# Performance work log

Measured on AMD Instinct MI355X. Metric: run time of the kernel, lower is better.

Reference implementation:

```python
import jax, jax.numpy as jnp
import numpy as np

N, E, G = 100000, 300000, 4096
ND, ED, H, ZI, ZS, NE, L = 64, 16, 256, 128, 128, 8, 3
LAMBDA_GRL = 1.0


def setup_inputs() -> dict:
    key = jax.random.key(0)
    ks = iter(jax.random.split(key, 64))
    def nrm(shape, scale=0.05):
        return jax.random.normal(next(ks), shape, jnp.float32) * scale
    inp = {
        'x': jax.random.normal(next(ks), (N, ND), jnp.float32),
        'edge_index': jax.random.randint(next(ks), (2, E), 0, N),
        'edge_attr': jax.random.normal(next(ks), (E, ED), jnp.float32),
        'batch': jnp.sort(jax.random.randint(next(ks), (N,), 0, G)),
        'node_W': nrm((ND, H)), 'node_b': nrm((H,)),
        'conv_eps': jnp.zeros((L,), jnp.float32),
        'edge_W': nrm((L, ED, H)), 'edge_b': nrm((L, H)),
        'mlp_W1': nrm((L, H, H)), 'mlp_b1': nrm((L, H)),
        'mlp_W2': nrm((L, H, H)), 'mlp_b2': nrm((L, H)),
        'gn_w': jnp.ones((L, H), jnp.float32), 'gn_b': jnp.zeros((L, H), jnp.float32),
        'gn_ms': jnp.ones((L, H), jnp.float32),
        'finv_W1': nrm((H, ZI)), 'finv_b1': nrm((ZI,)),
        'finv_W2': nrm((ZI, ZI)), 'finv_b2': nrm((ZI,)),
        'fspu_W1': nrm((H, ZS)), 'fspu_b1': nrm((ZS,)),
        'fspu_W2': nrm((ZS, ZS)), 'fspu_b2': nrm((ZS,)),
        'pred_W1': nrm((ZI, ZI)), 'pred_b1': nrm((ZI,)),
        'pred_W2': nrm((ZI, 1)), 'pred_b2': nrm((1,)),
        'adv_W1': nrm((ZI, ZI)), 'adv_b1': nrm((ZI,)),
        'adv_W2': nrm((ZI, NE)), 'adv_b2': nrm((NE,)),
    }
    return inp


def _mlp2(h, W1, b1, W2, b2):
    return jax.nn.relu(h @ W1 + b1) @ W2 + b2


def reference(x, edge_index, edge_attr, batch, node_W, node_b, conv_eps,
              edge_W, edge_b, mlp_W1, mlp_b1, mlp_W2, mlp_b2,
              gn_w, gn_b, gn_ms,
              finv_W1, finv_b1, finv_W2, finv_b2,
              fspu_W1, fspu_b1, fspu_W2, fspu_b2,
              pred_W1, pred_b1, pred_W2, pred_b2,
              adv_W1, adv_b1, adv_W2, adv_b2):
    src, dst = edge_index[0], edge_index[1]
    cnt = jax.ops.segment_sum(jnp.ones((N, 1), jnp.float32), batch, num_segments=G)
    cnt = jnp.maximum(cnt, 1.0)
    h = x @ node_W + node_b  # [N,H]
    for l in range(L):
        # GINEConv: sum_j relu(x_j + lin(e_ij))
        e = edge_attr @ edge_W[l] + edge_b[l]            # [E,H]
        m = jax.nn.relu(h[src] + e)                      # [E,H]
        agg = jax.ops.segment_sum(m, dst, num_segments=N)
        h = _mlp2((1.0 + conv_eps[l]) * h + agg, mlp_W1[l], mlp_b1[l], mlp_W2[l], mlp_b2[l])
        # GraphNorm
        mean = jax.ops.segment_sum(h, batch, num_segments=G) / cnt  # [G,H]
        out = h - gn_ms[l] * mean[batch]
        var = jax.ops.segment_sum(out * out, batch, num_segments=G) / cnt
        h = out * jax.lax.rsqrt(var[batch] + 1e-5) * gn_w[l] + gn_b[l]
        h = jax.nn.relu(h)  # dropout is identity at eval
    hg = jax.ops.segment_sum(h, batch, num_segments=G) / cnt  # global_mean_pool [G,H]
    z_inv = _mlp2(hg, finv_W1, finv_b1, finv_W2, finv_b2)
    z_spu = _mlp2(hg, fspu_W1, fspu_b1, fspu_W2, fspu_b2)
    yhat = _mlp2(z_inv, pred_W1, pred_b1, pred_W2, pred_b2)[:, 0]
    # gradient reversal: identity fwd, -lambda on bwd
    grl = jax.lax.stop_gradient(z_inv) * (1.0 + LAMBDA_GRL) - LAMBDA_GRL * z_inv
    envhat = _mlp2(grl, adv_W1, adv_b1, adv_W2, adv_b2)
    return (hg, z_inv, z_spu, yhat, envhat)
```

## Files before the change

kernel.cpp:

```cpp
#include <hip/hip_runtime.h>
#include <hip/hip_bf16.h>

typedef __bf16 bf16_t;
typedef __bf16 bf16x8 __attribute__((ext_vector_type(8)));
typedef __bf16 bf16x4 __attribute__((ext_vector_type(4)));
typedef float  f32x4  __attribute__((ext_vector_type(4)));

static constexpr int N_NODES = 100000;
static constexpr int N_EDGES = 300000;
static constexpr int N_GRAPH = 4096;
static constexpr int H  = 256;
static constexpr int ND = 64;
static constexpr int ZIC = 128;
static constexpr int NE = 8;
static constexpr int SCAN_B = 1024;

__device__ __forceinline__ int clampi(int v, int lo, int hi) {
  return v < lo ? lo : (v > hi ? hi : v);
}

__device__ __forceinline__ void dma16(const bf16_t* g, bf16_t* lds_base) {
  __builtin_amdgcn_global_load_lds(
      (const __attribute__((address_space(1))) void*)g,
      (__attribute__((address_space(3))) void*)lds_base, 16, 0, 0);
}

__global__ void compute_starts_kernel(const int* __restrict__ batch,
                                      int* __restrict__ starts, int N, int G) {
  int i = blockIdx.x * blockDim.x + threadIdx.x;
  if (i >= N) return;
  int b = clampi(batch[i], 0, G - 1);
  if (i == 0) {
    for (int g = 0; g <= b; ++g) starts[g] = 0;
  } else {
    int p = clampi(batch[i - 1], 0, G - 1);
    for (int g = p + 1; g <= b; ++g) starts[g] = i;
  }
  if (i == N - 1) {
    for (int g = b + 1; g <= G; ++g) starts[g] = N;
  }
}

__global__ void zero2_kernel(int* __restrict__ a, int* __restrict__ b, int N) {
  int i = blockIdx.x * blockDim.x + threadIdx.x;
  if (i < N) { a[i] = 0; b[i] = 0; }
}

__global__ void count_deg_kernel(const int* __restrict__ dst, int* __restrict__ counts, int E, int N) {
  int e = blockIdx.x * blockDim.x + threadIdx.x;
  if (e < E) atomicAdd(&counts[clampi(dst[e], 0, N - 1)], 1);
}

__global__ __launch_bounds__(SCAN_B) void scan1_kernel(const int* __restrict__ counts,
                                                       int* __restrict__ offs,
                                                       int* __restrict__ bsum, int N) {
  __shared__ int tmp[SCAN_B];
  int i = blockIdx.x * SCAN_B + threadIdx.x;
  int v = (i < N) ? counts[i] : 0;
  tmp[threadIdx.x] = v;
  __syncthreads();
  for (int d = 1; d < SCAN_B; d <<= 1) {
    int t = (threadIdx.x >= d) ? tmp[threadIdx.x - d] : 0;
    __syncthreads();
    tmp[threadIdx.x] += t;
    __syncthreads();
  }
  if (i < N) offs[i + 1] = tmp[threadIdx.x];
  if (threadIdx.x == SCAN_B - 1) bsum[blockIdx.x] = tmp[SCAN_B - 1];
  if (i == 0) offs[0] = 0;
}

__global__ void scan2_kernel(int* __restrict__ bsum, int nblk) {
  if (blockIdx.x == 0 && threadIdx.x == 0) {
    int run = 0;
    for (int b = 0; b < nblk; ++b) { int v = bsum[b]; bsum[b] = run; run += v; }
  }
}

__global__ __launch_bounds__(SCAN_B) void scan3_kernel(int* __restrict__ offs,
                                                       const int* __restrict__ bsum, int N) {
  int i = blockIdx.x * SCAN_B + threadIdx.x;
  if (i < N) offs[i + 1] += bsum[blockIdx.x];
}

__global__ void fill_perm_kernel(const int* __restrict__ dst, const int* __restrict__ offs,
                                 int* __restrict__ cursor, int* __restrict__ perm, int E, int N) {
  int e = blockIdx.x * blockDim.x + threadIdx.x;
  if (e >= E) return;
  int d = clampi(dst[e], 0, N - 1);
  int pos = offs[d] + atomicAdd(&cursor[d], 1);
  if ((unsigned)pos < (unsigned)E) perm[pos] = e;
}

__global__ void sort_src_kernel(const int* __restrict__ perm, const int* __restrict__ src,
                                int* __restrict__ src_sorted, int E) {
  int p = blockIdx.x * blockDim.x + threadIdx.x;
  if (p >= E) return;
  int e = perm[p];
  e = ((unsigned)e < (unsigned)E) ? e : 0;
  int s = src[e];
  src_sorted[p] = ((unsigned)s < (unsigned)N_NODES) ? s : 0;
}

__global__ void build_eattr16_kernel(const float* __restrict__ eattr,
                                     const int* __restrict__ perm,
                                     bf16_t* __restrict__ ep, int E) {
  int idx = blockIdx.x * blockDim.x + threadIdx.x;
  if (idx >= E * 16) return;
  int p = idx >> 4, k = idx & 15;
  int e = perm[p];
  e = ((unsigned)e < (unsigned)E) ? e : 0;
  ep[idx] = (bf16_t)eattr[(size_t)e * 16 + k];
}

__global__ void build_ewt16_kernel(const float* __restrict__ edge_W,
                                   bf16_t* __restrict__ ewt) {
  int idx = blockIdx.x * blockDim.x + threadIdx.x;
  if (idx >= 3 * 256 * 16) return;
  int l = idx / (256 * 16);
  int rem = idx - l * 256 * 16;
  int n = rem >> 4, k = rem & 15;
  ewt[idx] = (bf16_t)edge_W[(size_t)l * 16 * 256 + k * 256 + n];
}

__global__ void transpose_kernel(const float* __restrict__ W,
                                 bf16_t* __restrict__ Wt, int K, int Nc) {
  __shared__ float tile[32][33];
  int n0 = blockIdx.x * 32, k0 = blockIdx.y * 32;
  int tx = threadIdx.x, ty = threadIdx.y;
  for (int i = ty; i < 32; i += 8)
    tile[i][tx] = W[(size_t)(k0 + i) * Nc + n0 + tx];
  __syncthreads();
  for (int i = ty; i < 32; i += 8)
    Wt[(size_t)(n0 + i) * K + k0 + tx] = (bf16_t)tile[tx][i];
}

__device__ __forceinline__ void load8_to_lds(const bf16_t* p, bool valid, uint4* dst) {
  uint4 v = make_uint4(0u, 0u, 0u, 0u);
  if (valid) v = *(const uint4*)p;
  *dst = v;
}
__device__ __forceinline__ void load8_to_lds(const float* p, bool valid, uint4* dst) {
  float4 f0 = make_float4(0.f, 0.f, 0.f, 0.f), f1 = f0;
  if (valid) { f0 = *(const float4*)p; f1 = *(const float4*)(p + 4); }
  union { bf16_t b[8]; uint4 u; } pk;
  pk.b[0] = (bf16_t)f0.x; pk.b[1] = (bf16_t)f0.y;
  pk.b[2] = (bf16_t)f0.z; pk.b[3] = (bf16_t)f0.w;
  pk.b[4] = (bf16_t)f1.x; pk.b[5] = (bf16_t)f1.y;
  pk.b[6] = (bf16_t)f1.z; pk.b[7] = (bf16_t)f1.w;
  *dst = pk.u;
}

template<int K, bool RELU, bool OUTF32, typename TIN>
__global__ __launch_bounds__(256) void gemm128_kernel(
    const TIN* __restrict__ U, const bf16_t* __restrict__ Wt,
    const float* __restrict__ bias, void* __restrict__ Out, int M, int Nc) {
  constexpr int LDT = 72;
  __shared__ bf16_t Ut[128 * LDT];
  __shared__ bf16_t Wl[128 * LDT];
  const int m0 = blockIdx.x * 128;
  const int n0 = blockIdx.y * 128;
  const int t = threadIdx.x;
  const int lane = t & 63;
  const int wave = t >> 6;
  const int wm = (wave >> 1) * 64;
  const int wn = (wave & 1) * 64;
  const int srow = t >> 1;
  const int sk = (t & 1) * 32;
  const int lr = lane & 15;
  const int lq = lane >> 4;
  const bool aok = (m0 + srow) < M;
  f32x4 acc[4][4] = {};

  for (int k0 = 0; k0 < K; k0 += 64) {
    const TIN* up = U + (size_t)(m0 + srow) * K + k0 + sk;
    const bf16_t* wp = Wt + (size_t)(n0 + srow) * K + k0 + sk;
#pragma unroll
    for (int q = 0; q < 4; ++q) {
      load8_to_lds(up + q * 8, aok, (uint4*)&Ut[srow * LDT + sk + q * 8]);
      load8_to_lds(wp + q * 8, true, (uint4*)&Wl[srow * LDT + sk + q * 8]);
    }
    __syncthreads();
#pragma unroll
    for (int s = 0; s < 2; ++s) {
      bf16x8 a[4], b[4];
#pragma unroll
      for (int mt = 0; mt < 4; ++mt)
        a[mt] = *(const bf16x8*)(&Ut[(wm + mt * 16 + lr) * LDT + s * 32 + lq * 8]);
#pragma unroll
      for (int nt = 0; nt < 4; ++nt)
        b[nt] = *(const bf16x8*)(&Wl[(wn + nt * 16 + lr) * LDT + s * 32 + lq * 8]);
#pragma unroll
      for (int mt = 0; mt < 4; ++mt)
#pragma unroll
        for (int nt = 0; nt < 4; ++nt)
          acc[mt][nt] = __builtin_amdgcn_mfma_f32_16x16x32_bf16(
              a[mt], b[nt], acc[mt][nt], 0, 0, 0);
    }
    __syncthreads();
  }

#pragma unroll
  for (int mt = 0; mt < 4; ++mt)
#pragma unroll
    for (int nt = 0; nt < 4; ++nt) {
      int col = n0 + wn + nt * 16 + lr;
      float bcol = bias[col];
#pragma unroll
      for (int r = 0; r < 4; ++r) {
        int row = m0 + wm + mt * 16 + lq * 4 + r;
        if (row < M) {
          float vv = acc[mt][nt][r] + bcol;
          if (RELU) vv = vv > 0.f ? vv : 0.f;
          if (OUTF32) ((float*)Out)[(size_t)row * Nc + col] = vv;
          else        ((bf16_t*)Out)[(size_t)row * Nc + col] = (bf16_t)vv;
        }
      }
    }
}

template<int K, bool RELU, bool OUTF32, typename TIN>
__global__ __launch_bounds__(256) void gemm64_kernel(
    const TIN* __restrict__ U, const bf16_t* __restrict__ Wt,
    const float* __restrict__ bias, void* __restrict__ Out, int M, int Nc) {
  constexpr int LDT = 72;
  __shared__ bf16_t Ut[64 * LDT];
  __shared__ bf16_t Wl[64 * LDT];
  const int m0 = blockIdx.x * 64;
  const int n0 = blockIdx.y * 64;
  const int t = threadIdx.x;
  const int lane = t & 63;
  const int wave = t >> 6;
  const int wm = (wave >> 1) * 32;
  const int wn = (wave & 1) * 32;
  const int srow = t >> 2;
  const int sk = (t & 3) * 8;
  const int lr = lane & 15;
  const int lq = lane >> 4;
  const bool aok = (m0 + srow) < M;
  f32x4 acc[2][2] = {};

  for (int k0 = 0; k0 < K; k0 += 64) {
    const TIN* up = U + (size_t)(m0 + srow) * K + k0 + sk;
    const bf16_t* wp = Wt + (size_t)(n0 + srow) * K + k0 + sk;
    load8_to_lds(up,      aok, (uint4*)&Ut[srow * LDT + sk]);
    load8_to_lds(up + 32, aok, (uint4*)&Ut[srow * LDT + sk + 32]);
    load8_to_lds(wp,      true, (uint4*)&Wl[srow * LDT + sk]);
    load8_to_lds(wp + 32, true, (uint4*)&Wl[srow * LDT + sk + 32]);
    __syncthreads();
#pragma unroll
    for (int s = 0; s < 2; ++s) {
      bf16x8 a[2], b[2];
#pragma unroll
      for (int mt = 0; mt < 2; ++mt)
        a[mt] = *(const bf16x8*)(&Ut[(wm + mt * 16 + lr) * LDT + s * 32 + lq * 8]);
#pragma unroll
      for (int nt = 0; nt < 2; ++nt)
        b[nt] = *(const bf16x8*)(&Wl[(wn + nt * 16 + lr) * LDT + s * 32 + lq * 8]);
#pragma unroll
      for (int mt = 0; mt < 2; ++mt)
#pragma unroll
        for (int nt = 0; nt < 2; ++nt)
          acc[mt][nt] = __builtin_amdgcn_mfma_f32_16x16x32_bf16(
              a[mt], b[nt], acc[mt][nt], 0, 0, 0);
    }
    __syncthreads();
  }

#pragma unroll
  for (int mt = 0; mt < 2; ++mt)
#pragma unroll
    for (int nt = 0; nt < 2; ++nt) {
      int col = n0 + wn + nt * 16 + lr;
      float bcol = bias[col];
#pragma unroll
      for (int r = 0; r < 4; ++r) {
        int row = m0 + wm + mt * 16 + lq * 4 + r;
        if (row < M) {
          float vv = acc[mt][nt][r] + bcol;
          if (RELU) vv = vv > 0.f ? vv : 0.f;
          if (OUTF32) ((float*)Out)[(size_t)row * Nc + col] = vv;
          else        ((bf16_t*)Out)[(size_t)row * Nc + col] = (bf16_t)vv;
        }
      }
    }
}

template<int K, bool RELU, bool OUTF32>
__global__ __launch_bounds__(256) void gemm128_dma_kernel(
    const bf16_t* __restrict__ U, const bf16_t* __restrict__ Wt,
    const float* __restrict__ bias, void* __restrict__ Out, int M, int Nc) {
  __shared__ bf16_t Ut[128 * 64];
  __shared__ bf16_t Wl[128 * 64];
  const int t = threadIdx.x;
  const int lane = t & 63;
  const int wave = t >> 6;
  const int m0 = blockIdx.x * 128;
  const int n0 = blockIdx.y * 128;
  const int wm = (wave >> 1) * 64;
  const int wn = (wave & 1) * 64;
  const int lr = lane & 15;
  const int lq = lane >> 4;
  const int subrow = wave * 8 + (lane >> 3);
  const int lchunk = (lane & 7) ^ (lane >> 3);
  f32x4 acc[4][4] = {};

  for (int k0 = 0; k0 < K; k0 += 64) {
#pragma unroll
    for (int q = 0; q < 4; ++q) {
      const int row = q * 32 + subrow;
      int urow = m0 + row; if (urow >= M) urow = M - 1;
      dma16(U + (size_t)urow * K + k0 + lchunk * 8, &Ut[(q * 32 + wave * 8) * 64]);
      dma16(Wt + (size_t)(n0 + row) * K + k0 + lchunk * 8, &Wl[(q * 32 + wave * 8) * 64]);
    }
    __syncthreads();
#pragma unroll
    for (int s = 0; s < 2; ++s) {
      bf16x8 a[4], b[4];
#pragma unroll
      for (int mt = 0; mt < 4; ++mt)
        a[mt] = *(const bf16x8*)(&Ut[(wm + mt * 16 + lr) * 64 + (((s * 4 + lq) ^ (lr & 7)) << 3)]);
#pragma unroll
      for (int nt = 0; nt < 4; ++nt)
        b[nt] = *(const bf16x8*)(&Wl[(wn + nt * 16 + lr) * 64 + (((s * 4 + lq) ^ (lr & 7)) << 3)]);
#pragma unroll
      for (int mt = 0; mt < 4; ++mt)
#pragma unroll
        for (int nt = 0; nt < 4; ++nt)
          acc[mt][nt] = __builtin_amdgcn_mfma_f32_16x16x32_bf16(
              a[mt], b[nt], acc[mt][nt], 0, 0, 0);
    }
    __syncthreads();
  }

#pragma unroll
  for (int mt = 0; mt < 4; ++mt)
#pragma unroll
    for (int nt = 0; nt < 4; ++nt) {
      int col = n0 + wn + nt * 16 + lr;
      float bcol = bias[col];
#pragma unroll
      for (int r = 0; r < 4; ++r) {
        int row = m0 + wm + mt * 16 + lq * 4 + r;
        if (row < M) {
          float vv = acc[mt][nt][r] + bcol;
          if (RELU) vv = vv > 0.f ? vv : 0.f;
          if (OUTF32) ((float*)Out)[(size_t)row * Nc + col] = vv;
          else        ((bf16_t*)Out)[(size_t)row * Nc + col] = (bf16_t)vv;
        }
      }
    }
}

__global__ __launch_bounds__(256) void gine_gather_mfma_kernel(
    const bf16_t* __restrict__ h, const bf16_t* __restrict__ eat16,
    const int* __restrict__ src_sorted, const int* __restrict__ offs,
    const bf16_t* __restrict__ ewt, const float* __restrict__ eb,
    const float* __restrict__ eps_p, bf16_t* __restrict__ u) {
  constexpr int HP = H + 8;
  __shared__ bf16_t slin[2][16 * HP];
  const int t = threadIdx.x;
  const int wave = t >> 6;
  const int lane = t & 63;
  const int lr = lane & 15;
  const int lq = lane >> 4;
  const int lane4 = lane * 4;
  const int n0 = blockIdx.x * 4;
  const int nodeN = n0 + wave;

  bf16x4 hs = *(const bf16x4*)(h + (size_t)nodeN * H + lane4);

  bf16x8 bfrag[4];
#pragma unroll
  for (int nt = 0; nt < 4; ++nt) {
    bf16x8 bv = {};
    if (lq < 2)
      bv = *(const bf16x8*)(ewt + ((wave * 64 + nt * 16 + lr) << 4) + (lq << 3));
    bfrag[nt] = bv;
  }
  float ebv[4];
#pragma unroll
  for (int i = 0; i < 4; ++i) ebv[i] = eb[lane4 + i];

  int bs = offs[n0], be = offs[n0 + 4];
  bs = clampi(bs, 0, N_EDGES);
  be = clampi(be, bs, N_EDGES);
  int ns = offs[nodeN], ne = offs[nodeN + 1];
  ns = clampi(ns, bs, be);
  ne = clampi(ne, ns, be);

  float acc[4] = {0.f, 0.f, 0.f, 0.f};
  int parity = 0;

  for (int cb = bs; cb < be; cb += 16, parity ^= 1) {
    int arow = cb + lr;
    if (arow >= N_EDGES) arow = N_EDGES - 1;
    bf16x8 afrag = {};
    if (lq < 2)
      afrag = *(const bf16x8*)(eat16 + ((size_t)arow << 4) + (lq << 3));
    f32x4 c[4];
#pragma unroll
    for (int nt = 0; nt < 4; ++nt) {
      f32x4 z = {};
      c[nt] = __builtin_amdgcn_mfma_f32_16x16x32_bf16(afrag, bfrag[nt], z, 0, 0, 0);
    }
#pragma unroll
    for (int nt = 0; nt < 4; ++nt)
#pragma unroll
      for (int r = 0; r < 4; ++r)
        slin[parity][(lq * 4 + r) * HP + wave * 64 + nt * 16 + lr] = (bf16_t)c[nt][r];
    __syncthreads();
    int j0 = ns > cb ? ns : cb;
    int j1 = ne < cb + 16 ? ne : cb + 16;
    for (int jb = j0; jb < j1; jb += 4) {
      int sidx[4];
#pragma unroll
      for (int q = 0; q < 4; ++q) {
        int jj = jb + q; if (jj > j1 - 1) jj = j1 - 1;
        sidx[q] = src_sorted[jj];
      }
      bf16x4 hv[4];
#pragma unroll
      for (int q = 0; q < 4; ++q)
        hv[q] = *(const bf16x4*)(h + (size_t)sidx[q] * H + lane4);
#pragma unroll
      for (int q = 0; q < 4; ++q) {
        if (jb + q < j1) {
          bf16x4 lv = *(const bf16x4*)(&slin[parity][(jb + q - cb) * HP + lane4]);
#pragma unroll
          for (int i = 0; i < 4; ++i)
            acc[i] += fmaxf((float)hv[q][i] + (float)lv[i] + ebv[i], 0.f);
        }
      }
    }
  }

  const float sc = 1.0f + eps_p[0];
  union { bf16x4 v; uint2 b; } o;
#pragma unroll
  for (int i = 0; i < 4; ++i) o.v[i] = (bf16_t)(sc * (float)hs[i] + acc[i]);
  *(uint2*)(u + (size_t)nodeN * H + lane4) = o.b;
}

__global__ __launch_bounds__(64) void graphnorm_kernel(
    const bf16_t* __restrict__ v, bf16_t* __restrict__ hout,
    const int* __restrict__ starts,
    const float* __restrict__ w, const float* __restrict__ b,
    const float* __restrict__ ms, float* __restrict__ hg) {
  const int g = blockIdx.x;
  const int c0 = threadIdx.x * 4;
  int s = starts[g], e = starts[g + 1];
  s = clampi(s, 0, N_NODES);
  e = clampi(e, s, N_NODES);
  const float cnt = (float)((e - s) > 1 ? (e - s) : 1);
  float sx[4] = {0.f, 0.f, 0.f, 0.f}, sxx[4] = {0.f, 0.f, 0.f, 0.f};
  for (int i = s; i < e; ++i) {
    bf16x4 xv = *(const bf16x4*)(v + (size_t)i * H + c0);
#pragma unroll
    for (int j = 0; j < 4; ++j) { float f = (float)xv[j]; sx[j] += f; sxx[j] += f * f; }
  }
  float sub[4], inv[4], bb[4], psum[4] = {0.f, 0.f, 0.f, 0.f};
#pragma unroll
  for (int j = 0; j < 4; ++j) {
    float mean = sx[j] / cnt;
    sub[j] = ms[c0 + j] * mean;
    float var = sxx[j] / cnt - 2.f * sub[j] * mean + sub[j] * sub[j];
    var = fmaxf(var, 0.f);
    inv[j] = rsqrtf(var + 1e-5f) * w[c0 + j];
    bb[j] = b[c0 + j];
  }
  for (int i = s; i < e; ++i) {
    bf16x4 xv = *(const bf16x4*)(v + (size_t)i * H + c0);
    union { bf16x4 o; uint2 u; } pk;
#pragma unroll
    for (int j = 0; j < 4; ++j) {
      float o = ((float)xv[j] - sub[j]) * inv[j] + bb[j];
      o = o > 0.f ? o : 0.f;
      psum[j] += o;
      pk.o[j] = (bf16_t)o;
    }
    *(uint2*)(hout + (size_t)i * H + c0) = pk.u;
  }
  if (hg) {
#pragma unroll
    for (int j = 0; j < 4; ++j) hg[(size_t)g * H + c0 + j] = psum[j] / cnt;
  }
}

__global__ void head_out_kernel(const bf16_t* __restrict__ In, const float* __restrict__ W,
                                const float* __restrict__ bias, float* __restrict__ Out,
                                int M, int K, int Nc) {
  int idx = blockIdx.x * blockDim.x + threadIdx.x;
  if (idx >= M * Nc) return;
  int r = idx / Nc, n = idx - r * Nc;
  float acc = bias[n];
  const bf16_t* in = In + (size_t)r * K;
  for (int k = 0; k < K; ++k) acc += (float)in[k] * W[(size_t)k * Nc + n];
  Out[idx] = acc;
}

extern "C" void kernel_launch(void* const* d_in, const int* in_sizes, int n_in,
                              void* d_out, int out_size, void* d_ws, size_t ws_size,
                              hipStream_t stream) {
  (void)in_sizes; (void)n_in; (void)out_size; (void)ws_size;
  const float* x        = (const float*)d_in[0];
  const int*   eidx     = (const int*)d_in[1];
  const float* eattr    = (const float*)d_in[2];
  const int*   batch    = (const int*)d_in[3];
  const float* node_W   = (const float*)d_in[4];
  const float* node_b   = (const float*)d_in[5];
  const float* conv_eps = (const float*)d_in[6];
  const float* edge_W   = (const float*)d_in[7];
  const float* edge_b   = (const float*)d_in[8];
  const float* mlp_W1   = (const float*)d_in[9];
  const float* mlp_b1   = (const float*)d_in[10];
  const float* mlp_W2   = (const float*)d_in[11];
  const float* mlp_b2   = (const float*)d_in[12];
  const float* gn_w     = (const float*)d_in[13];
  const float* gn_b     = (const float*)d_in[14];
  const float* gn_ms    = (const float*)d_in[15];
  const float* finv_W1  = (const float*)d_in[16];
  const float* finv_b1  = (const float*)d_in[17];
  const float* finv_W2  = (const float*)d_in[18];
  const float* finv_b2  = (const float*)d_in[19];
  const float* fspu_W1  = (const float*)d_in[20];
  const float* fspu_b1  = (const float*)d_in[21];
  const float* fspu_W2  = (const float*)d_in[22];
  const float* fspu_b2  = (const float*)d_in[23];
  const float* pred_W1  = (const float*)d_in[24];
  const float* pred_b1  = (const float*)d_in[25];
  const float* pred_W2  = (const float*)d_in[26];
  const float* pred_b2  = (const float*)d_in[27];
  const float* adv_W1   = (const float*)d_in[28];
  const float* adv_b1   = (const float*)d_in[29];
  const float* adv_W2   = (const float*)d_in[30];
  const float* adv_b2   = (const float*)d_in[31];
  float* out = (float*)d_out;

  float* out_hg = out;
  float* out_zi = out + (size_t)N_GRAPH * H;
  float* out_zs = out_zi + (size_t)N_GRAPH * ZIC;
  float* out_yh = out_zs + (size_t)N_GRAPH * ZIC;
  float* out_ev = out_yh + N_GRAPH;

  char* wp = (char*)d_ws;
  auto alloc = [&](size_t bytes) { char* p = wp; wp += (bytes + 255) & ~(size_t)255; return p; };
  bf16_t* A        = (bf16_t*)alloc((size_t)N_NODES * H * 2);
  bf16_t* B        = (bf16_t*)alloc((size_t)N_NODES * H * 2);
  bf16_t* Wt       = (bf16_t*)alloc((size_t)(H * ND + 6 * H * H) * 2);
  bf16_t* WtH      = (bf16_t*)alloc((size_t)(2 * ZIC * H + 4 * ZIC * ZIC) * 2);
  bf16_t* ewt16    = (bf16_t*)alloc((size_t)3 * 256 * 16 * 2);
  bf16_t* eat16    = (bf16_t*)alloc((size_t)N_EDGES * 16 * 2);
  int*    starts   = (int*)alloc((size_t)(N_GRAPH + 1) * 4);
  int*    counts   = (int*)alloc((size_t)N_NODES * 4);
  int*    cursor   = (int*)alloc((size_t)N_NODES * 4);
  int*    offs     = (int*)alloc((size_t)(N_NODES + 1) * 4);
  int*    bsum     = (int*)alloc((size_t)SCAN_B * 4);
  int*    perm     = (int*)alloc((size_t)N_EDGES * 4);
  int*    src_srt  = (int*)alloc((size_t)N_EDGES * 4);
  bf16_t* tmp1     = (bf16_t*)alloc((size_t)N_GRAPH * ZIC * 2);
  bf16_t* tmp2     = (bf16_t*)alloc((size_t)N_GRAPH * ZIC * 2);

  const int* srcp = eidx;
  const int* dstp = eidx + N_EDGES;
  const int nscan = (N_NODES + SCAN_B - 1) / SCAN_B;

  compute_starts_kernel<<<(N_NODES + 255) / 256, 256, 0, stream>>>(batch, starts, N_NODES, N_GRAPH);

  zero2_kernel<<<(N_NODES + 255) / 256, 256, 0, stream>>>(counts, cursor, N_NODES);
  count_deg_kernel<<<(N_EDGES + 255) / 256, 256, 0, stream>>>(dstp, counts, N_EDGES, N_NODES);
  scan1_kernel<<<nscan, SCAN_B, 0, stream>>>(counts, offs, bsum, N_NODES);
  scan2_kernel<<<1, 64, 0, stream>>>(bsum, nscan);
  scan3_kernel<<<nscan, SCAN_B, 0, stream>>>(offs, bsum, N_NODES);
  fill_perm_kernel<<<(N_EDGES + 255) / 256, 256, 0, stream>>>(dstp, offs, cursor, perm, N_EDGES, N_NODES);
  sort_src_kernel<<<(N_EDGES + 255) / 256, 256, 0, stream>>>(perm, srcp, src_srt, N_EDGES);
  build_eattr16_kernel<<<(N_EDGES * 16 + 255) / 256, 256, 0, stream>>>(eattr, perm, eat16, N_EDGES);
  build_ewt16_kernel<<<(3 * 256 * 16 + 255) / 256, 256, 0, stream>>>(edge_W, ewt16);

  bf16_t* WtN = Wt;
  auto Wt1l = [&](int l) { return Wt + H * ND + (size_t)(2 * l) * H * H; };
  auto Wt2l = [&](int l) { return Wt + H * ND + (size_t)(2 * l + 1) * H * H; };
  transpose_kernel<<<dim3(H / 32, ND / 32), dim3(32, 8), 0, stream>>>(node_W, WtN, ND, H);
  for (int l = 0; l < 3; ++l) {
    transpose_kernel<<<dim3(H / 32, H / 32), dim3(32, 8), 0, stream>>>(mlp_W1 + (size_t)l * H * H, Wt1l(l), H, H);
    transpose_kernel<<<dim3(H / 32, H / 32), dim3(32, 8), 0, stream>>>(mlp_W2 + (size_t)l * H * H, Wt2l(l), H, H);
  }
  bf16_t* fT1 = WtH;
  bf16_t* fT2 = fT1 + ZIC * H;
  bf16_t* sT1 = fT2 + ZIC * ZIC;
  bf16_t* sT2 = sT1 + ZIC * H;
  bf16_t* pT1 = sT2 + ZIC * ZIC;
  bf16_t* aT1 = pT1 + ZIC * ZIC;
  transpose_kernel<<<dim3(ZIC / 32, H / 32), dim3(32, 8), 0, stream>>>(finv_W1, fT1, H, ZIC);
  transpose_kernel<<<dim3(ZIC / 32, ZIC / 32), dim3(32, 8), 0, stream>>>(finv_W2, fT2, ZIC, ZIC);
  transpose_kernel<<<dim3(ZIC / 32, H / 32), dim3(32, 8), 0, stream>>>(fspu_W1, sT1, H, ZIC);
  transpose_kernel<<<dim3(ZIC / 32, ZIC / 32), dim3(32, 8), 0, stream>>>(fspu_W2, sT2, ZIC, ZIC);
  transpose_kernel<<<dim3(ZIC / 32, ZIC / 32), dim3(32, 8), 0, stream>>>(pred_W1, pT1, ZIC, ZIC);
  transpose_kernel<<<dim3(ZIC / 32, ZIC / 32), dim3(32, 8), 0, stream>>>(adv_W1, aT1, ZIC, ZIC);

  dim3 ggrid((N_NODES + 127) / 128, H / 128);
  gemm128_kernel<ND, false, false><<<ggrid, 256, 0, stream>>>(x, WtN, node_b, A, N_NODES, H);

  for (int l = 0; l < 3; ++l) {
    gine_gather_mfma_kernel<<<N_NODES / 4, 256, 0, stream>>>(
        A, eat16, src_srt, offs, ewt16 + (size_t)l * 256 * 16,
        edge_b + l * H, conv_eps + l, B);
    gemm128_dma_kernel<H, true,  false><<<ggrid, 256, 0, stream>>>(B, Wt1l(l), mlp_b1 + l * H, A, N_NODES, H);
    gemm128_dma_kernel<H, false, false><<<ggrid, 256, 0, stream>>>(A, Wt2l(l), mlp_b2 + l * H, B, N_NODES, H);
    graphnorm_kernel<<<N_GRAPH, 64, 0, stream>>>(B, A, starts, gn_w + l * H, gn_b + l * H,
                                                 gn_ms + l * H, (l == 2) ? out_hg : nullptr);
  }

  dim3 hgrid(N_GRAPH / 64, ZIC / 64);
  gemm64_kernel<H,   true,  false, float ><<<hgrid, 256, 0, stream>>>(out_hg, fT1, finv_b1, tmp1, N_GRAPH, ZIC);
  gemm64_kernel<ZIC, false, true,  bf16_t><<<hgrid, 256, 0, stream>>>(tmp1, fT2, finv_b2, out_zi, N_GRAPH, ZIC);
  gemm64_kernel<H,   true,  false, float ><<<hgrid, 256, 0, stream>>>(out_hg, sT1, fspu_b1, tmp2, N_GRAPH, ZIC);
  gemm64_kernel<ZIC, false, true,  bf16_t><<<hgrid, 256, 0, stream>>>(tmp2, sT2, fspu_b2, out_zs, N_GRAPH, ZIC);
  gemm64_kernel<ZIC, true,  false, float ><<<hgrid, 256, 0, stream>>>(out_zi, pT1, pred_b1, tmp1, N_GRAPH, ZIC);
  gemm64_kernel<ZIC, true,  false, float ><<<hgrid, 256, 0, stream>>>(out_zi, aT1, adv_b1, tmp2, N_GRAPH, ZIC);
  head_out_kernel<<<(N_GRAPH + 255) / 256, 256, 0, stream>>>(tmp1, pred_W2, pred_b2, out_yh, N_GRAPH, ZIC, 1);
  head_out_kernel<<<(N_GRAPH * NE + 255) / 256, 256, 0, stream>>>(tmp2, adv_W2, adv_b2, out_ev, N_GRAPH, ZIC, NE);
}
```

Before: 854.7 us.

## Fuse edge sort scatter kernels, batch weight transposes, unroll graphnorm loops

The three CSR-build kernels (perm fill, src gather, edge-attr gather) become one kernel that writes src and bf16 edge attributes directly at the sorted position. This removes the perm buffer and two launches. The per-layer weight transposes are batched into single launches over blockIdx.z. Graphnorm's two row loops are unrolled by four so several loads are in flight per thread. The atomic ordering within a node's edge segment is nondeterministic in both versions, so results are unchanged.

```diff
diff --git a/kernel.cpp b/kernel.cpp
--- a/kernel.cpp
+++ b/kernel.cpp
@@ -83,34 +83,25 @@
   if (i < N) offs[i + 1] += bsum[blockIdx.x];
 }
 
-__global__ void fill_perm_kernel(const int* __restrict__ dst, const int* __restrict__ offs,
-                                 int* __restrict__ cursor, int* __restrict__ perm, int E, int N) {
+__global__ void fill_scatter_kernel(const int* __restrict__ src, const int* __restrict__ dst,
+                                    const float* __restrict__ eattr,
+                                    const int* __restrict__ offs, int* __restrict__ cursor,
+                                    int* __restrict__ src_srt, bf16_t* __restrict__ eat16,
+                                    int E, int N) {
   int e = blockIdx.x * blockDim.x + threadIdx.x;
   if (e >= E) return;
   int d = clampi(dst[e], 0, N - 1);
   int pos = offs[d] + atomicAdd(&cursor[d], 1);
-  if ((unsigned)pos < (unsigned)E) perm[pos] = e;
-}
-
-__global__ void sort_src_kernel(const int* __restrict__ perm, const int* __restrict__ src,
-                                int* __restrict__ src_sorted, int E) {
-  int p = blockIdx.x * blockDim.x + threadIdx.x;
-  if (p >= E) return;
-  int e = perm[p];
-  e = ((unsigned)e < (unsigned)E) ? e : 0;
+  if ((unsigned)pos >= (unsigned)E) return;
   int s = src[e];
-  src_sorted[p] = ((unsigned)s < (unsigned)N_NODES) ? s : 0;
-}
-
-__global__ void build_eattr16_kernel(const float* __restrict__ eattr,
-                                     const int* __restrict__ perm,
-                                     bf16_t* __restrict__ ep, int E) {
-  int idx = blockIdx.x * blockDim.x + threadIdx.x;
-  if (idx >= E * 16) return;
-  int p = idx >> 4, k = idx & 15;
-  int e = perm[p];
-  e = ((unsigned)e < (unsigned)E) ? e : 0;
-  ep[idx] = (bf16_t)eattr[(size_t)e * 16 + k];
+  src_srt[pos] = ((unsigned)s < (unsigned)N_NODES) ? s : 0;
+  const float* ea = eattr + (size_t)e * 16;
+  union { bf16_t b[16]; uint4 u[2]; } pk;
+#pragma unroll
+  for (int k = 0; k < 16; ++k) pk.b[k] = (bf16_t)ea[k];
+  uint4* dst16 = (uint4*)(eat16 + ((size_t)pos << 4));
+  dst16[0] = pk.u[0];
+  dst16[1] = pk.u[1];
 }
 
 __global__ void build_ewt16_kernel(const float* __restrict__ edge_W,
@@ -124,15 +115,18 @@
 }
 
 __global__ void transpose_kernel(const float* __restrict__ W,
-                                 bf16_t* __restrict__ Wt, int K, int Nc) {
+                                 bf16_t* __restrict__ Wt, int K, int Nc,
+                                 size_t srcStride, size_t dstStride) {
   __shared__ float tile[32][33];
+  const float* Wz = W + (size_t)blockIdx.z * srcStride;
+  bf16_t* Wtz = Wt + (size_t)blockIdx.z * dstStride;
   int n0 = blockIdx.x * 32, k0 = blockIdx.y * 32;
   int tx = threadIdx.x, ty = threadIdx.y;
   for (int i = ty; i < 32; i += 8)
-    tile[i][tx] = W[(size_t)(k0 + i) * Nc + n0 + tx];
+    tile[i][tx] = Wz[(size_t)(k0 + i) * Nc + n0 + tx];
   __syncthreads();
   for (int i = ty; i < 32; i += 8)
-    Wt[(size_t)(n0 + i) * K + k0 + tx] = (bf16_t)tile[tx][i];
+    Wtz[(size_t)(n0 + i) * K + k0 + tx] = (bf16_t)tile[tx][i];
 }
 
 __device__ __forceinline__ void load8_to_lds(const bf16_t* p, bool valid, uint4* dst) {
@@ -454,7 +448,18 @@
   e = clampi(e, s, N_NODES);
   const float cnt = (float)((e - s) > 1 ? (e - s) : 1);
   float sx[4] = {0.f, 0.f, 0.f, 0.f}, sxx[4] = {0.f, 0.f, 0.f, 0.f};
-  for (int i = s; i < e; ++i) {
+  int i = s;
+  for (; i + 4 <= e; i += 4) {
+    bf16x4 xv[4];
+#pragma unroll
+    for (int q = 0; q < 4; ++q)
+      xv[q] = *(const bf16x4*)(v + (size_t)(i + q) * H + c0);
+#pragma unroll
+    for (int q = 0; q < 4; ++q)
+#pragma unroll
+      for (int j = 0; j < 4; ++j) { float f = (float)xv[q][j]; sx[j] += f; sxx[j] += f * f; }
+  }
+  for (; i < e; ++i) {
     bf16x4 xv = *(const bf16x4*)(v + (size_t)i * H + c0);
 #pragma unroll
     for (int j = 0; j < 4; ++j) { float f = (float)xv[j]; sx[j] += f; sxx[j] += f * f; }
@@ -469,7 +474,26 @@
     inv[j] = rsqrtf(var + 1e-5f) * w[c0 + j];
     bb[j] = b[c0 + j];
   }
-  for (int i = s; i < e; ++i) {
+  i = s;
+  for (; i + 4 <= e; i += 4) {
+    bf16x4 xv[4];
+#pragma unroll
+    for (int q = 0; q < 4; ++q)
+      xv[q] = *(const bf16x4*)(v + (size_t)(i + q) * H + c0);
+#pragma unroll
+    for (int q = 0; q < 4; ++q) {
+      union { bf16x4 o; uint2 u; } pk;
+#pragma unroll
+      for (int j = 0; j < 4; ++j) {
+        float o = ((float)xv[q][j] - sub[j]) * inv[j] + bb[j];
+        o = o > 0.f ? o : 0.f;
+        psum[j] += o;
+        pk.o[j] = (bf16_t)o;
+      }
+      *(uint2*)(hout + (size_t)(i + q) * H + c0) = pk.u;
+    }
+  }
+  for (; i < e; ++i) {
     bf16x4 xv = *(const bf16x4*)(v + (size_t)i * H + c0);
     union { bf16x4 o; uint2 u; } pk;
 #pragma unroll
@@ -556,7 +580,6 @@
   int*    cursor   = (int*)alloc((size_t)N_NODES * 4);
   int*    offs     = (int*)alloc((size_t)(N_NODES + 1) * 4);
   int*    bsum     = (int*)alloc((size_t)SCAN_B * 4);
-  int*    perm     = (int*)alloc((size_t)N_EDGES * 4);
   int*    src_srt  = (int*)alloc((size_t)N_EDGES * 4);
   bf16_t* tmp1     = (bf16_t*)alloc((size_t)N_GRAPH * ZIC * 2);
   bf16_t* tmp2     = (bf16_t*)alloc((size_t)N_GRAPH * ZIC * 2);
@@ -572,31 +595,33 @@
   scan1_kernel<<<nscan, SCAN_B, 0, stream>>>(counts, offs, bsum, N_NODES);
   scan2_kernel<<<1, 64, 0, stream>>>(bsum, nscan);
   scan3_kernel<<<nscan, SCAN_B, 0, stream>>>(offs, bsum, N_NODES);
-  fill_perm_kernel<<<(N_EDGES + 255) / 256, 256, 0, stream>>>(dstp, offs, cursor, perm, N_EDGES, N_NODES);
-  sort_src_kernel<<<(N_EDGES + 255) / 256, 256, 0, stream>>>(perm, srcp, src_srt, N_EDGES);
-  build_eattr16_kernel<<<(N_EDGES * 16 + 255) / 256, 256, 0, stream>>>(eattr, perm, eat16, N_EDGES);
+  fill_scatter_kernel<<<(N_EDGES + 255) / 256, 256, 0, stream>>>(
+      srcp, dstp, eattr, offs, cursor, src_srt, eat16, N_EDGES, N_NODES);
   build_ewt16_kernel<<<(3 * 256 * 16 + 255) / 256, 256, 0, stream>>>(edge_W, ewt16);
 
   bf16_t* WtN = Wt;
-  auto Wt1l = [&](int l) { return Wt + H * ND + (size_t)(2 * l) * H * H; };
-  auto Wt2l = [&](int l) { return Wt + H * ND + (size_t)(2 * l + 1) * H * H; };
-  transpose_kernel<<<dim3(H / 32, ND / 32), dim3(32, 8), 0, stream>>>(node_W, WtN, ND, H);
-  for (int l = 0; l < 3; ++l) {
-    transpose_kernel<<<dim3(H / 32, H / 32), dim3(32, 8), 0, stream>>>(mlp_W1 + (size_t)l * H * H, Wt1l(l), H, H);
-    transpose_kernel<<<dim3(H / 32, H / 32), dim3(32, 8), 0, stream>>>(mlp_W2 + (size_t)l * H * H, Wt2l(l), H, H);
-  }
+  bf16_t* Wt1base = Wt + H * ND;
+  bf16_t* Wt2base = Wt + H * ND + (size_t)H * H;
+  auto Wt1l = [&](int l) { return Wt1base + (size_t)(2 * l) * H * H; };
+  auto Wt2l = [&](int l) { return Wt2base + (size_t)(2 * l) * H * H; };
+  transpose_kernel<<<dim3(H / 32, ND / 32, 1), dim3(32, 8), 0, stream>>>(node_W, WtN, ND, H, 0, 0);
+  transpose_kernel<<<dim3(H / 32, H / 32, 3), dim3(32, 8), 0, stream>>>(
+      mlp_W1, Wt1base, H, H, (size_t)H * H, (size_t)2 * H * H);
+  transpose_kernel<<<dim3(H / 32, H / 32, 3), dim3(32, 8), 0, stream>>>(
+      mlp_W2, Wt2base, H, H, (size_t)H * H, (size_t)2 * H * H);
+
   bf16_t* fT1 = WtH;
   bf16_t* fT2 = fT1 + ZIC * H;
   bf16_t* sT1 = fT2 + ZIC * ZIC;
   bf16_t* sT2 = sT1 + ZIC * H;
   bf16_t* pT1 = sT2 + ZIC * ZIC;
   bf16_t* aT1 = pT1 + ZIC * ZIC;
-  transpose_kernel<<<dim3(ZIC / 32, H / 32), dim3(32, 8), 0, stream>>>(finv_W1, fT1, H, ZIC);
-  transpose_kernel<<<dim3(ZIC / 32, ZIC / 32), dim3(32, 8), 0, stream>>>(finv_W2, fT2, ZIC, ZIC);
-  transpose_kernel<<<dim3(ZIC / 32, H / 32), dim3(32, 8), 0, stream>>>(fspu_W1, sT1, H, ZIC);
-  transpose_kernel<<<dim3(ZIC / 32, ZIC / 32), dim3(32, 8), 0, stream>>>(fspu_W2, sT2, ZIC, ZIC);
-  transpose_kernel<<<dim3(ZIC / 32, ZIC / 32), dim3(32, 8), 0, stream>>>(pred_W1, pT1, ZIC, ZIC);
-  transpose_kernel<<<dim3(ZIC / 32, ZIC / 32), dim3(32, 8), 0, stream>>>(adv_W1, aT1, ZIC, ZIC);
+  transpose_kernel<<<dim3(ZIC / 32, H / 32, 1), dim3(32, 8), 0, stream>>>(finv_W1, fT1, H, ZIC, 0, 0);
+  transpose_kernel<<<dim3(ZIC / 32, ZIC / 32, 1), dim3(32, 8), 0, stream>>>(finv_W2, fT2, ZIC, ZIC, 0, 0);
+  transpose_kernel<<<dim3(ZIC / 32, H / 32, 1), dim3(32, 8), 0, stream>>>(fspu_W1, sT1, H, ZIC, 0, 0);
+  transpose_kernel<<<dim3(ZIC / 32, ZIC / 32, 1), dim3(32, 8), 0, stream>>>(fspu_W2, sT2, ZIC, ZIC, 0, 0);
+  transpose_kernel<<<dim3(ZIC / 32, ZIC / 32, 1), dim3(32, 8), 0, stream>>>(pred_W1, pT1, ZIC, ZIC, 0, 0);
+  transpose_kernel<<<dim3(ZIC / 32, ZIC / 32, 1), dim3(32, 8), 0, stream>>>(adv_W1, aT1, ZIC, ZIC, 0, 0);
 
   dim3 ggrid((N_NODES + 127) / 128, H / 128);
   gemm128_kernel<ND, false, false><<<ggrid, 256, 0, stream>>>(x, WtN, node_b, A, N_NODES, H);
```

Result: faster. 817.1 us (-4.4%).
